# Performance work log

Measured on AMD Instinct MI355X. Metric: run time of the kernel, lower is better.

## Reference

```python
import jax, jax.numpy as jnp
from jax import lax
import numpy as np

B, N, H = 8, 2048, 128
THRESH = 0.3


def setup_inputs() -> dict:
    key = jax.random.key(0)
    k1, k2, k3 = jax.random.split(key, 3)
    node_embeddings = jax.random.normal(k1, (B * N, H), jnp.float32)
    # contiguous equal-sized graphs, as produced by PyG-style batching
    batch = jnp.repeat(jnp.arange(B, dtype=jnp.int64), N)
    # path_scorer params: Linear(2H->H) then Linear(H->1)
    W1 = jax.random.normal(k2, (2 * H, H), jnp.float32) * 0.02  # input-major
    b1 = jnp.zeros((H,), jnp.float32)
    W2 = jax.random.normal(k3, (H,), jnp.float32) * 0.02
    b2 = jnp.zeros((), jnp.float32)
    return {"node_embeddings": node_embeddings, "batch": batch,
            "W1": W1, "b1": b1, "W2": W2, "b2": b2}


def _run(emb, W1, b1, W2, b2):
    """emb: [B, N, H]. Returns (path [B,N] int32 padded with -1, scores [B,N])."""
    Bn, Nn, Hh = emb.shape
    bidx = jnp.arange(Bn)
    nidx = jnp.arange(Nn)
    # split first Linear: score(i,j) = sigmoid(w2 . elu(e_i@W1a + e_j@W1b + b1) + b2)
    A = jnp.einsum('bnh,hk->bnk', emb, W1[:Hh])          # current-node half [B,N,H]
    C = jnp.einsum('bnh,hk->bnk', emb, W1[Hh:]) + b1     # neighbor half + bias [B,N,H]
    root = jnp.argmax(emb[:, :, 0], axis=1)              # [B]
    visited0 = jnp.zeros((Bn, Nn), bool).at[bidx, root].set(True)

    def step(carry, _):
        cur, visited, active = carry
        # score every node against the current node in one fused pass
        h = jax.nn.elu(A[bidx, cur][:, None, :] + C)                      # [B,N,H]
        s = jax.nn.sigmoid(jnp.einsum('bnh,h->bn', h, W2) + b2)           # [B,N]
        sm = jnp.where(visited, -jnp.inf, s)
        best = jnp.argmax(sm, axis=1)                                     # first max == stable sort
        bscore = jnp.take_along_axis(sm, best[:, None], axis=1)[:, 0]
        take = active & (bscore > THRESH)
        visited = visited | (take[:, None] & (nidx[None, :] == best[:, None]))
        new_cur = jnp.where(take, best, cur)
        step_path = jnp.where(take, best, -1).astype(jnp.int32)
        step_score = jnp.where(take, bscore, 0.0).astype(emb.dtype)
        return (new_cur, visited, take), (step_path, step_score)

    init = (root, visited0, jnp.ones((Bn,), bool))
    _, (paths, scoreseq) = lax.scan(step, init, None, length=Nn - 1)
    path = jnp.concatenate([root[:, None].astype(jnp.int32), paths.T], axis=1)      # [B,N]
    scores = jnp.concatenate([jnp.ones((Bn, 1), emb.dtype), scoreseq.T], axis=1)    # root score = 1.0
    return path, scores


def reference(node_embeddings, batch, W1, b1, W2, b2):
    num_graphs = int(batch[-1]) + 1  # contiguous equal-sized graphs
    emb = node_embeddings.reshape(num_graphs, -1, node_embeddings.shape[-1])
    return _run(emb, W1, b1, W2, b2)
```

## Files before the change

kernel.cpp:

```cpp
#include <hip/hip_runtime.h>
#include <math.h>

#define B_ 8
#define N_ 2048
#define H_ 128
#define BN_ (B_ * N_)


__device__ __forceinline__ float elu1(float x) {
    return x > 0.f ? x : (__expf(x) - 1.f);
}

__device__ __forceinline__ unsigned enc_key(float v) {
    unsigned u = __float_as_uint(v);
    return (u & 0x80000000u) ? ~u : (u | 0x80000000u);
}
__device__ __forceinline__ float dec_key(unsigned k) {
    return __uint_as_float((k & 0x80000000u) ? (k & 0x7FFFFFFFu) : ~k);
}

__global__ __launch_bounds__(H_) void k_ac(const float* __restrict__ emb,
                                           const float* __restrict__ W1,
                                           const float* __restrict__ b1,
                                           float* __restrict__ A,
                                           float* __restrict__ C) {
    __shared__ float e[H_];
    const int i = blockIdx.x;
    const int k = threadIdx.x;
    e[k] = emb[(size_t)i * H_ + k];
    __syncthreads();
    float a = 0.f, c = 0.f;
#pragma unroll 8
    for (int h = 0; h < H_; ++h) {
        const float ev = e[h];
        a = fmaf(ev, W1[h * H_ + k], a);
        c = fmaf(ev, W1[(H_ + h) * H_ + k], c);
    }
    A[(size_t)i * H_ + k] = a;
    C[(size_t)i * H_ + k] = c + b1[k];
}

__global__ __launch_bounds__(256) void k_z(const float* __restrict__ A,
                                           const float* __restrict__ Cc,
                                           const float* __restrict__ w2,
                                           const float* __restrict__ b2p,
                                           unsigned* __restrict__ K) {
    const int lane = threadIdx.x & 63;
    const int wave = threadIdx.x >> 6;
    const int g = blockIdx.x >> 8;
    const int sub = blockIdx.x & 255;
    const int rowtile = sub & 127;
    const int jh = sub >> 7;
    const int ibase = rowtile * 16 + wave * 4;
    const int i = ibase + (lane & 3);
    const int he = (lane >> 2) * 8;
    const float b2v = *b2p;

    const float* Arow = A + ((size_t)g * N_ + i) * H_ + he;
    const float4 a0 = *(const float4*)(Arow);
    const float4 a1 = *(const float4*)(Arow + 4);
    const float4 w0 = *(const float4*)(w2 + he);
    const float4 w1v = *(const float4*)(w2 + he + 4);
    const float* Cg = Cc + (size_t)g * N_ * H_ + he;
    unsigned* Krow = K + ((size_t)g * N_ + i) * N_;
    const bool writer = ((lane >> 2) == 0);

    const int j0 = jh * 1024;
    for (int j = j0; j < j0 + 1024; j += 8) {
        float4 c0[8], c1[8];
#pragma unroll
        for (int q = 0; q < 8; ++q) {
            const float* Cj = Cg + (size_t)(j + q) * H_;
            c0[q] = *(const float4*)(Cj);
            c1[q] = *(const float4*)(Cj + 4);
        }
        float pv[8];
#pragma unroll
        for (int q = 0; q < 8; ++q) {
            float p = 0.f;
            p = fmaf(w0.x, elu1(a0.x + c0[q].x), p);
            p = fmaf(w0.y, elu1(a0.y + c0[q].y), p);
            p = fmaf(w0.z, elu1(a0.z + c0[q].z), p);
            p = fmaf(w0.w, elu1(a0.w + c0[q].w), p);
            p = fmaf(w1v.x, elu1(a1.x + c1[q].x), p);
            p = fmaf(w1v.y, elu1(a1.y + c1[q].y), p);
            p = fmaf(w1v.z, elu1(a1.z + c1[q].z), p);
            p = fmaf(w1v.w, elu1(a1.w + c1[q].w), p);
            pv[q] = p;
        }
#pragma unroll
        for (int q = 0; q < 8; ++q) pv[q] += __shfl_xor(pv[q], 4);
#pragma unroll
        for (int q = 0; q < 8; ++q) pv[q] += __shfl_xor(pv[q], 8);
#pragma unroll
        for (int q = 0; q < 8; ++q) pv[q] += __shfl_xor(pv[q], 16);
#pragma unroll
        for (int q = 0; q < 8; ++q) pv[q] += __shfl_xor(pv[q], 32);
        if (writer) {
            uint4 ka, kb;
            ka.x = enc_key(pv[0] + b2v);
            ka.y = enc_key(pv[1] + b2v);
            ka.z = enc_key(pv[2] + b2v);
            ka.w = enc_key(pv[3] + b2v);
            kb.x = enc_key(pv[4] + b2v);
            kb.y = enc_key(pv[5] + b2v);
            kb.z = enc_key(pv[6] + b2v);
            kb.w = enc_key(pv[7] + b2v);
            *(uint4*)(Krow + j) = ka;
            *(uint4*)(Krow + j + 4) = kb;
        }
    }
}

__global__ __launch_bounds__(64, 1) void k_path5(const float* __restrict__ emb,
                                                 const unsigned* __restrict__ K,
                                                 float* __restrict__ out) {
    const int g = blockIdx.x;
    const int lane = threadIdx.x;

    float bv0 = -INFINITY;
    int bi0 = 0x7fffffff;
    for (int j = lane; j < N_; j += 64) {
        const float v = emb[((size_t)g * N_ + j) * H_];
        if (v > bv0) { bv0 = v; bi0 = j; }
    }
#pragma unroll
    for (int off = 1; off < 64; off <<= 1) {
        const float ov = __shfl_xor(bv0, off);
        const int oi = __shfl_xor(bi0, off);
        if (ov > bv0 || (ov == bv0 && oi < bi0)) { bv0 = ov; bi0 = oi; }
    }
    int cur = bi0;
    unsigned vbits = 0;
    if (((cur >> 2) & 63) == lane)
        vbits |= 1u << (((cur >> 8) << 2) | (cur & 3));

    float* pathOut = out + (size_t)g * N_;
    float* scoreOut = out + (size_t)BN_ + (size_t)g * N_;
    if (lane == 0) {
        pathOut[0] = (float)cur;
        scoreOut[0] = 1.0f;
    }

    const unsigned* Kg = K + (size_t)g * N_ * N_;
    uint4 z[8];
    {
        const uint4* Kr = (const uint4*)(Kg + ((size_t)cur << 11));
#pragma unroll
        for (int k = 0; k < 8; ++k) z[k] = Kr[k * 64 + lane];
    }

    int t = 1;
    for (; t < N_; ++t) {
        unsigned best = 0u;
        int bj = 0;
#define SLOT(KRAW, S)                                                   \
        {                                                               \
            const unsigned kv_ = ((vbits >> (S)) & 1u) ? 0u : (KRAW);   \
            if (kv_ >= best) { best = kv_; bj = (S); }                  \
        }
        SLOT(z[7].w, 31) SLOT(z[7].z, 30) SLOT(z[7].y, 29) SLOT(z[7].x, 28)
        SLOT(z[6].w, 27) SLOT(z[6].z, 26) SLOT(z[6].y, 25) SLOT(z[6].x, 24)
        SLOT(z[5].w, 23) SLOT(z[5].z, 22) SLOT(z[5].y, 21) SLOT(z[5].x, 20)
        SLOT(z[4].w, 19) SLOT(z[4].z, 18) SLOT(z[4].y, 17) SLOT(z[4].x, 16)
        SLOT(z[3].w, 15) SLOT(z[3].z, 14) SLOT(z[3].y, 13) SLOT(z[3].x, 12)
        SLOT(z[2].w, 11) SLOT(z[2].z, 10) SLOT(z[2].y,  9) SLOT(z[2].x,  8)
        SLOT(z[1].w,  7) SLOT(z[1].z,  6) SLOT(z[1].y,  5) SLOT(z[1].x,  4)
        SLOT(z[0].w,  3) SLOT(z[0].z,  2) SLOT(z[0].y,  1) SLOT(z[0].x,  0)
#undef SLOT

        unsigned w = best;
#pragma unroll
        for (int off = 1; off < 64; off <<= 1) {
            const unsigned ow = __shfl_xor(w, off);
            if (ow > w) w = ow;
        }
        const unsigned long long mk = __ballot(best == w);
        int bi;
        if (__popcll(mk) == 1) {
            const int src = (int)(__ffsll((long long)mk) - 1);
            const int bjw = __shfl(bj, src);
            bi = ((bjw >> 2) << 8) | (src << 2) | (bjw & 3);
        } else {
            unsigned cand = (best == w)
                ? ~(unsigned)(((bj >> 2) << 8) | (lane << 2) | (bj & 3))
                : 0u;
#pragma unroll
            for (int off = 1; off < 64; off <<= 1) {
                const unsigned oc = __shfl_xor(cand, off);
                if (oc > cand) cand = oc;
            }
            bi = (int)(~cand);
        }

        {
            const uint4* Kr = (const uint4*)(Kg + ((size_t)bi << 11));
#pragma unroll
            for (int k = 0; k < 8; ++k) z[k] = Kr[k * 64 + lane];
        }

        const float bv = dec_key(w);
        const float s = 1.f / (1.f + expf(-bv));
        if (!((double)s > 0.3)) break;
        cur = bi;
        if (((cur >> 2) & 63) == lane)
            vbits |= 1u << (((cur >> 8) << 2) | (cur & 3));
        if (lane == 0) {
            pathOut[t] = (float)cur;
            scoreOut[t] = s;
        }
    }
    for (int tt = t + lane; tt < N_; tt += 64) {
        pathOut[tt] = -1.f;
        scoreOut[tt] = 0.f;
    }
}

__device__ __forceinline__ void blockArgmax(float& bv, int& bi, float* rv, int* ri,
                                            int lane, int wid, int nw) {
#pragma unroll
    for (int off = 1; off < 64; off <<= 1) {
        const float ov = __shfl_xor(bv, off);
        const int oi = __shfl_xor(bi, off);
        if (ov > bv || (ov == bv && oi < bi)) { bv = ov; bi = oi; }
    }
    if (lane == 0) { rv[wid] = bv; ri[wid] = bi; }
    __syncthreads();
    if (wid == 0) {
        float v = (lane < nw) ? rv[lane] : -INFINITY;
        int ix = (lane < nw) ? ri[lane] : 0x7fffffff;
#pragma unroll
        for (int off = 1; off < 16; off <<= 1) {
            const float ov = __shfl_xor(v, off);
            const int oi = __shfl_xor(ix, off);
            if (ov > v || (ov == v && oi < ix)) { v = ov; ix = oi; }
        }
        if (lane == 0) { rv[0] = v; ri[0] = ix; }
    }
    __syncthreads();
    bv = rv[0];
    bi = ri[0];
}

__global__ __launch_bounds__(1024) void k_path_fly(const float* __restrict__ emb,
                                                   const float* __restrict__ A,
                                                   const float* __restrict__ Cc,
                                                   const float* __restrict__ w2g,
                                                   const float* __restrict__ b2p,
                                                   float* __restrict__ out) {
    const int g = blockIdx.x;
    const int tid = threadIdx.x;
    const int lane = tid & 63, wid = tid >> 6;
    __shared__ float acur[H_], w2s[H_];
    __shared__ unsigned char vis[N_];
    __shared__ float rv[16];
    __shared__ int ri[16];
    const float b2v = *b2p;
    if (tid < H_) w2s[tid] = w2g[tid];
    for (int j = tid; j < N_; j += 1024) vis[j] = 0;

    float bv = -INFINITY;
    int bi = 0x7fffffff;
    for (int j = tid; j < N_; j += 1024) {
        const float v = emb[((size_t)g * N_ + j) * H_];
        if (v > bv) { bv = v; bi = j; }
    }
    __syncthreads();
    blockArgmax(bv, bi, rv, ri, lane, wid, 16);
    int cur = bi;
    float* pathOut = out + (size_t)g * N_;
    float* scoreOut = out + (size_t)BN_ + (size_t)g * N_;
    if (tid == 0) {
        vis[cur] = 1;
        pathOut[0] = (float)cur;
        scoreOut[0] = 1.0f;
    }
    __syncthreads();

    int t = 1;
    for (; t < N_; ++t) {
        if (tid < H_) acur[tid] = A[((size_t)g * N_ + cur) * H_ + tid];
        __syncthreads();
        float mbv = -INFINITY;
        int mbi = 0x7fffffff;
#pragma unroll
        for (int q = 0; q < 2; ++q) {
            const int j = tid + q * 1024;
            const float* Cj = Cc + ((size_t)g * N_ + j) * H_;
            float p = 0.f;
            for (int h = 0; h < H_; h += 4) {
                const float4 c = *(const float4*)(Cj + h);
                p = fmaf(w2s[h + 0], elu1(acur[h + 0] + c.x), p);
                p = fmaf(w2s[h + 1], elu1(acur[h + 1] + c.y), p);
                p = fmaf(w2s[h + 2], elu1(acur[h + 2] + c.z), p);
                p = fmaf(w2s[h + 3], elu1(acur[h + 3] + c.w), p);
            }
            const float z = p + b2v;
            if (!vis[j] && (z > mbv || (z == mbv && j < mbi))) { mbv = z; mbi = j; }
        }
        __syncthreads();
        blockArgmax(mbv, mbi, rv, ri, lane, wid, 16);
        const float s = 1.f / (1.f + expf(-mbv));
        if (!((double)s > 0.3)) break;
        cur = mbi;
        if (tid == 0) {
            vis[cur] = 1;
            pathOut[t] = (float)cur;
            scoreOut[t] = s;
        }
        __syncthreads();
    }
    for (int tt = t + tid; tt < N_; tt += 1024) {
        pathOut[tt] = -1.f;
        scoreOut[tt] = 0.f;
    }
}

extern "C" void kernel_launch(void* const* d_in, const int* in_sizes, int n_in,
                              void* d_out, int out_size, void* d_ws, size_t ws_size,
                              hipStream_t stream) {
    (void)in_sizes; (void)n_in; (void)out_size;
    const float* emb = (const float*)d_in[0];
    const float* W1 = (const float*)d_in[2];
    const float* b1 = (const float*)d_in[3];
    const float* w2 = (const float*)d_in[4];
    const float* b2 = (const float*)d_in[5];
    float* out = (float*)d_out;

    float* A = (float*)d_ws;
    float* C = A + (size_t)BN_ * H_;
    unsigned* K = (unsigned*)(C + (size_t)BN_ * H_);
    const size_t need = ((size_t)BN_ * H_ * 2 + (size_t)B_ * N_ * N_) * sizeof(float);

    hipLaunchKernelGGL(k_ac, dim3(BN_), dim3(H_), 0, stream, emb, W1, b1, A, C);
    if (ws_size >= need) {
        hipLaunchKernelGGL(k_z, dim3(2048), dim3(256), 0, stream, A, C, w2, b2, K);
        hipLaunchKernelGGL(k_path5, dim3(B_), dim3(64), 0, stream, emb, K, out);
    } else {
        hipLaunchKernelGGL(k_path_fly, dim3(B_), dim3(1024), 0, stream,
                           emb, A, C, w2, b2, out);
    }
}
```

Before: 3.218 ms.

## Fuse score-matrix build and path walk with per-row readiness flags

```diff
diff --git a/kernel.cpp b/kernel.cpp
--- a/kernel.cpp
+++ b/kernel.cpp
@@ -5,6 +5,7 @@
 #define N_ 2048
 #define H_ 128
 #define BN_ (B_ * N_)
+#define NZBLK_ 2048
 
 
 __device__ __forceinline__ float elu1(float x) {
@@ -18,6 +19,7 @@
 __device__ __forceinline__ float dec_key(unsigned k) {
     return __uint_as_float((k & 0x80000000u) ? (k & 0x7FFFFFFFu) : ~k);
 }
+__device__ __forceinline__ unsigned umax2(unsigned a, unsigned b) { return a > b ? a : b; }
 
 __global__ __launch_bounds__(H_) void k_ac(const float* __restrict__ emb,
                                            const float* __restrict__ W1,
@@ -40,81 +42,98 @@
     C[(size_t)i * H_ + k] = c + b1[k];
 }
 
-__global__ __launch_bounds__(256) void k_z(const float* __restrict__ A,
-                                           const float* __restrict__ Cc,
-                                           const float* __restrict__ w2,
-                                           const float* __restrict__ b2p,
-                                           unsigned* __restrict__ K) {
-    const int lane = threadIdx.x & 63;
-    const int wave = threadIdx.x >> 6;
-    const int g = blockIdx.x >> 8;
-    const int sub = blockIdx.x & 255;
-    const int rowtile = sub & 127;
-    const int jh = sub >> 7;
-    const int ibase = rowtile * 16 + wave * 4;
-    const int i = ibase + (lane & 3);
-    const int he = (lane >> 2) * 8;
-    const float b2v = *b2p;
-
-    const float* Arow = A + ((size_t)g * N_ + i) * H_ + he;
-    const float4 a0 = *(const float4*)(Arow);
-    const float4 a1 = *(const float4*)(Arow + 4);
-    const float4 w0 = *(const float4*)(w2 + he);
-    const float4 w1v = *(const float4*)(w2 + he + 4);
-    const float* Cg = Cc + (size_t)g * N_ * H_ + he;
-    unsigned* Krow = K + ((size_t)g * N_ + i) * N_;
-    const bool writer = ((lane >> 2) == 0);
-
-    const int j0 = jh * 1024;
-    for (int j = j0; j < j0 + 1024; j += 8) {
-        float4 c0[8], c1[8];
-#pragma unroll
-        for (int q = 0; q < 8; ++q) {
-            const float* Cj = Cg + (size_t)(j + q) * H_;
-            c0[q] = *(const float4*)(Cj);
-            c1[q] = *(const float4*)(Cj + 4);
-        }
-        float pv[8];
-#pragma unroll
-        for (int q = 0; q < 8; ++q) {
-            float p = 0.f;
-            p = fmaf(w0.x, elu1(a0.x + c0[q].x), p);
-            p = fmaf(w0.y, elu1(a0.y + c0[q].y), p);
-            p = fmaf(w0.z, elu1(a0.z + c0[q].z), p);
-            p = fmaf(w0.w, elu1(a0.w + c0[q].w), p);
-            p = fmaf(w1v.x, elu1(a1.x + c1[q].x), p);
-            p = fmaf(w1v.y, elu1(a1.y + c1[q].y), p);
-            p = fmaf(w1v.z, elu1(a1.z + c1[q].z), p);
-            p = fmaf(w1v.w, elu1(a1.w + c1[q].w), p);
-            pv[q] = p;
-        }
-#pragma unroll
-        for (int q = 0; q < 8; ++q) pv[q] += __shfl_xor(pv[q], 4);
-#pragma unroll
-        for (int q = 0; q < 8; ++q) pv[q] += __shfl_xor(pv[q], 8);
-#pragma unroll
-        for (int q = 0; q < 8; ++q) pv[q] += __shfl_xor(pv[q], 16);
-#pragma unroll
-        for (int q = 0; q < 8; ++q) pv[q] += __shfl_xor(pv[q], 32);
-        if (writer) {
-            uint4 ka, kb;
-            ka.x = enc_key(pv[0] + b2v);
-            ka.y = enc_key(pv[1] + b2v);
-            ka.z = enc_key(pv[2] + b2v);
-            ka.w = enc_key(pv[3] + b2v);
-            kb.x = enc_key(pv[4] + b2v);
-            kb.y = enc_key(pv[5] + b2v);
-            kb.z = enc_key(pv[6] + b2v);
-            kb.w = enc_key(pv[7] + b2v);
-            *(uint4*)(Krow + j) = ka;
-            *(uint4*)(Krow + j + 4) = kb;
-        }
-    }
-}
-
-__global__ __launch_bounds__(64, 1) void k_path5(const float* __restrict__ emb,
-                                                 const unsigned* __restrict__ K,
-                                                 float* __restrict__ out) {
+__global__ __launch_bounds__(256) void k_fused(const float* __restrict__ emb,
+                                               const float* __restrict__ A,
+                                               const float* __restrict__ Cc,
+                                               const float* __restrict__ w2,
+                                               const float* __restrict__ b2p,
+                                               unsigned* __restrict__ K,
+                                               unsigned* __restrict__ flags,
+                                               unsigned* __restrict__ gdone,
+                                               float* __restrict__ out) {
+    if (blockIdx.x >= B_) {
+        const int bid2 = blockIdx.x - B_;
+        const int lane = threadIdx.x & 63;
+        const int wave = threadIdx.x >> 6;
+        const int g = bid2 >> 8;
+        const int sub = bid2 & 255;
+        const int rowtile = sub & 127;
+        const int jh = sub >> 7;
+        const int ibase = rowtile * 16 + wave * 4;
+        const int i = ibase + (lane & 3);
+        const int he = (lane >> 2) * 8;
+        const float b2v = *b2p;
+
+        const float* Arow = A + ((size_t)g * N_ + i) * H_ + he;
+        const float4 a0 = *(const float4*)(Arow);
+        const float4 a1 = *(const float4*)(Arow + 4);
+        const float4 w0 = *(const float4*)(w2 + he);
+        const float4 w1v = *(const float4*)(w2 + he + 4);
+        const float* Cg = Cc + (size_t)g * N_ * H_ + he;
+        unsigned* Krow = K + ((size_t)g * N_ + i) * N_;
+        const bool writer = ((lane >> 2) == 0);
+
+        const int j0 = jh * 1024;
+        for (int j = j0; j < j0 + 1024; j += 8) {
+            float4 c0[8], c1[8];
+#pragma unroll
+            for (int q = 0; q < 8; ++q) {
+                const float* Cj = Cg + (size_t)(j + q) * H_;
+                c0[q] = *(const float4*)(Cj);
+                c1[q] = *(const float4*)(Cj + 4);
+            }
+            float pv[8];
+#pragma unroll
+            for (int q = 0; q < 8; ++q) {
+                float p = 0.f;
+                p = fmaf(w0.x, elu1(a0.x + c0[q].x), p);
+                p = fmaf(w0.y, elu1(a0.y + c0[q].y), p);
+                p = fmaf(w0.z, elu1(a0.z + c0[q].z), p);
+                p = fmaf(w0.w, elu1(a0.w + c0[q].w), p);
+                p = fmaf(w1v.x, elu1(a1.x + c1[q].x), p);
+                p = fmaf(w1v.y, elu1(a1.y + c1[q].y), p);
+                p = fmaf(w1v.z, elu1(a1.z + c1[q].z), p);
+                p = fmaf(w1v.w, elu1(a1.w + c1[q].w), p);
+                pv[q] = p;
+            }
+#pragma unroll
+            for (int q = 0; q < 8; ++q) pv[q] += __shfl_xor(pv[q], 4);
+#pragma unroll
+            for (int q = 0; q < 8; ++q) pv[q] += __shfl_xor(pv[q], 8);
+#pragma unroll
+            for (int q = 0; q < 8; ++q) pv[q] += __shfl_xor(pv[q], 16);
+#pragma unroll
+            for (int q = 0; q < 8; ++q) pv[q] += __shfl_xor(pv[q], 32);
+            if (writer) {
+                uint4 ka, kb;
+                ka.x = enc_key(pv[0] + b2v);
+                ka.y = enc_key(pv[1] + b2v);
+                ka.z = enc_key(pv[2] + b2v);
+                ka.w = enc_key(pv[3] + b2v);
+                kb.x = enc_key(pv[4] + b2v);
+                kb.y = enc_key(pv[5] + b2v);
+                kb.z = enc_key(pv[6] + b2v);
+                kb.w = enc_key(pv[7] + b2v);
+                *(uint4*)(Krow + j) = ka;
+                *(uint4*)(Krow + j + 4) = kb;
+            }
+        }
+
+        __threadfence();
+        __syncthreads();
+        if (threadIdx.x < 16) {
+            __hip_atomic_fetch_add(&flags[g * N_ + rowtile * 16 + threadIdx.x], 1u,
+                                   __ATOMIC_RELEASE, __HIP_MEMORY_SCOPE_AGENT);
+        }
+        __syncthreads();
+        if (threadIdx.x == 0) {
+            __hip_atomic_fetch_add(&gdone[g], 1u,
+                                   __ATOMIC_RELEASE, __HIP_MEMORY_SCOPE_AGENT);
+        }
+        return;
+    }
+
+    if (threadIdx.x >= 64) return;
     const int g = blockIdx.x;
     const int lane = threadIdx.x;
 
@@ -142,8 +161,22 @@
         scoreOut[0] = 1.0f;
     }
 
+    bool allReady = false;
+    const unsigned* fg = flags + (size_t)g * N_;
+    auto waitRow = [&](int r) {
+        if (allReady) return;
+        if (__hip_atomic_load(&gdone[g], __ATOMIC_ACQUIRE,
+                              __HIP_MEMORY_SCOPE_AGENT) == 256u) {
+            allReady = true;
+            return;
+        }
+        while (__hip_atomic_load(&fg[r], __ATOMIC_ACQUIRE,
+                                 __HIP_MEMORY_SCOPE_AGENT) < 2u) {}
+    };
+
     const unsigned* Kg = K + (size_t)g * N_ * N_;
     uint4 z[8];
+    waitRow(cur);
     {
         const uint4* Kr = (const uint4*)(Kg + ((size_t)cur << 11));
 #pragma unroll
@@ -193,6 +226,7 @@
             bi = (int)(~cand);
         }
 
+        waitRow(bi);
         {
             const uint4* Kr = (const uint4*)(Kg + ((size_t)bi << 11));
 #pragma unroll
@@ -330,12 +364,16 @@
     float* A = (float*)d_ws;
     float* C = A + (size_t)BN_ * H_;
     unsigned* K = (unsigned*)(C + (size_t)BN_ * H_);
-    const size_t need = ((size_t)BN_ * H_ * 2 + (size_t)B_ * N_ * N_) * sizeof(float);
+    unsigned* flags = K + (size_t)B_ * N_ * N_;
+    unsigned* gdone = flags + (size_t)BN_;
+    const size_t need = ((size_t)BN_ * H_ * 2 + (size_t)B_ * N_ * N_) * sizeof(float)
+                        + ((size_t)BN_ + B_) * sizeof(unsigned);
 
     hipLaunchKernelGGL(k_ac, dim3(BN_), dim3(H_), 0, stream, emb, W1, b1, A, C);
     if (ws_size >= need) {
-        hipLaunchKernelGGL(k_z, dim3(2048), dim3(256), 0, stream, A, C, w2, b2, K);
-        hipLaunchKernelGGL(k_path5, dim3(B_), dim3(64), 0, stream, emb, K, out);
+        hipMemsetAsync((void*)flags, 0, ((size_t)BN_ + B_) * sizeof(unsigned), stream);
+        hipLaunchKernelGGL(k_fused, dim3(B_ + NZBLK_), dim3(256), 0, stream,
+                           emb, A, C, w2, b2, K, flags, gdone, out);
     } else {
         hipLaunchKernelGGL(k_path_fly, dim3(B_), dim3(1024), 0, stream,
                            emb, A, C, w2, b2, out);
```

New measurement: 3.586 ms. 11.4% more time.

## Split sequential path argmax across four waves and use nontemporal loads for C

Applied to the files above, without the earlier changes.

```diff
diff --git a/kernel.cpp b/kernel.cpp
--- a/kernel.cpp
+++ b/kernel.cpp
@@ -6,6 +6,8 @@
 #define H_ 128
 #define BN_ (B_ * N_)
 
+
+typedef float f4v __attribute__((ext_vector_type(4)));
 
 __device__ __forceinline__ float elu1(float x) {
     return x > 0.f ? x : (__expf(x) - 1.f);
@@ -67,12 +69,12 @@
 
     const int j0 = jh * 1024;
     for (int j = j0; j < j0 + 1024; j += 8) {
-        float4 c0[8], c1[8];
+        f4v c0[8], c1[8];
 #pragma unroll
         for (int q = 0; q < 8; ++q) {
             const float* Cj = Cg + (size_t)(j + q) * H_;
-            c0[q] = *(const float4*)(Cj);
-            c1[q] = *(const float4*)(Cj + 4);
+            c0[q] = __builtin_nontemporal_load((const f4v*)(Cj));
+            c1[q] = __builtin_nontemporal_load((const f4v*)(Cj + 4));
         }
         float pv[8];
 #pragma unroll
@@ -112,105 +114,122 @@
     }
 }
 
-__global__ __launch_bounds__(64, 1) void k_path5(const float* __restrict__ emb,
-                                                 const unsigned* __restrict__ K,
-                                                 float* __restrict__ out) {
+__global__ __launch_bounds__(256) void k_path7(const float* __restrict__ emb,
+                                               const unsigned* __restrict__ K,
+                                               float* __restrict__ out) {
     const int g = blockIdx.x;
-    const int lane = threadIdx.x;
-
-    float bv0 = -INFINITY;
-    int bi0 = 0x7fffffff;
-    for (int j = lane; j < N_; j += 64) {
-        const float v = emb[((size_t)g * N_ + j) * H_];
-        if (v > bv0) { bv0 = v; bi0 = j; }
-    }
-#pragma unroll
-    for (int off = 1; off < 64; off <<= 1) {
-        const float ov = __shfl_xor(bv0, off);
-        const int oi = __shfl_xor(bi0, off);
-        if (ov > bv0 || (ov == bv0 && oi < bi0)) { bv0 = ov; bi0 = oi; }
-    }
-    int cur = bi0;
-    unsigned vbits = 0;
-    if (((cur >> 2) & 63) == lane)
-        vbits |= 1u << (((cur >> 8) << 2) | (cur & 3));
+    const int tid = threadIdx.x;
+    const int lane = tid & 63;
+    const int wid = tid >> 6;
+
+    __shared__ unsigned swv[2][4];
+    __shared__ int swj[2][4];
+    __shared__ int s_root;
 
     float* pathOut = out + (size_t)g * N_;
     float* scoreOut = out + (size_t)BN_ + (size_t)g * N_;
-    if (lane == 0) {
-        pathOut[0] = (float)cur;
-        scoreOut[0] = 1.0f;
-    }
+
+    if (tid < 64) {
+        float bv0 = -INFINITY;
+        int bi0 = 0x7fffffff;
+        for (int j = lane; j < N_; j += 64) {
+            const float v = emb[((size_t)g * N_ + j) * H_];
+            if (v > bv0) { bv0 = v; bi0 = j; }
+        }
+#pragma unroll
+        for (int off = 1; off < 64; off <<= 1) {
+            const float ov = __shfl_xor(bv0, off);
+            const int oi = __shfl_xor(bi0, off);
+            if (ov > bv0 || (ov == bv0 && oi < bi0)) { bv0 = ov; bi0 = oi; }
+        }
+        if (lane == 0) {
+            s_root = bi0;
+            pathOut[0] = (float)bi0;
+            scoreOut[0] = 1.0f;
+        }
+    }
+    __syncthreads();
+
+    int cur = s_root;
+    unsigned vb = 0;
+    if ((cur >> 3) == tid) vb |= 1u << (cur & 7);
 
     const unsigned* Kg = K + (size_t)g * N_ * N_;
-    uint4 z[8];
+    uint4 k0, k1;
     {
-        const uint4* Kr = (const uint4*)(Kg + ((size_t)cur << 11));
-#pragma unroll
-        for (int k = 0; k < 8; ++k) z[k] = Kr[k * 64 + lane];
-    }
-
+        const uint4* p = (const uint4*)(Kg + ((size_t)cur << 11) + (tid << 3));
+        k0 = p[0];
+        k1 = p[1];
+    }
+
+    int par = 0;
     int t = 1;
     for (; t < N_; ++t) {
-        unsigned best = 0u;
-        int bj = 0;
-#define SLOT(KRAW, S)                                                   \
-        {                                                               \
-            const unsigned kv_ = ((vbits >> (S)) & 1u) ? 0u : (KRAW);   \
-            if (kv_ >= best) { best = kv_; bj = (S); }                  \
-        }
-        SLOT(z[7].w, 31) SLOT(z[7].z, 30) SLOT(z[7].y, 29) SLOT(z[7].x, 28)
-        SLOT(z[6].w, 27) SLOT(z[6].z, 26) SLOT(z[6].y, 25) SLOT(z[6].x, 24)
-        SLOT(z[5].w, 23) SLOT(z[5].z, 22) SLOT(z[5].y, 21) SLOT(z[5].x, 20)
-        SLOT(z[4].w, 19) SLOT(z[4].z, 18) SLOT(z[4].y, 17) SLOT(z[4].x, 16)
-        SLOT(z[3].w, 15) SLOT(z[3].z, 14) SLOT(z[3].y, 13) SLOT(z[3].x, 12)
-        SLOT(z[2].w, 11) SLOT(z[2].z, 10) SLOT(z[2].y,  9) SLOT(z[2].x,  8)
-        SLOT(z[1].w,  7) SLOT(z[1].z,  6) SLOT(z[1].y,  5) SLOT(z[1].x,  4)
-        SLOT(z[0].w,  3) SLOT(z[0].z,  2) SLOT(z[0].y,  1) SLOT(z[0].x,  0)
-#undef SLOT
-
-        unsigned w = best;
+        const unsigned v0 = (vb & 1u)   ? 0u : k0.x;
+        const unsigned v1 = (vb & 2u)   ? 0u : k0.y;
+        const unsigned v2 = (vb & 4u)   ? 0u : k0.z;
+        const unsigned v3 = (vb & 8u)   ? 0u : k0.w;
+        const unsigned v4 = (vb & 16u)  ? 0u : k1.x;
+        const unsigned v5 = (vb & 32u)  ? 0u : k1.y;
+        const unsigned v6 = (vb & 64u)  ? 0u : k1.z;
+        const unsigned v7 = (vb & 128u) ? 0u : k1.w;
+
+        unsigned va = v0; int ja = 0;
+        if (v1 > va) { va = v1; ja = 1; }
+        unsigned vbp = v2; int jb = 2;
+        if (v3 > vbp) { vbp = v3; jb = 3; }
+        unsigned vc = v4; int jc = 4;
+        if (v5 > vc) { vc = v5; jc = 5; }
+        unsigned vd = v6; int jd = 6;
+        if (v7 > vd) { vd = v7; jd = 7; }
+        if (vbp > va) { va = vbp; ja = jb; }
+        if (vd > vc) { vc = vd; jc = jd; }
+        if (vc > va) { va = vc; ja = jc; }
+        unsigned wv_ = va;
+        int wj_ = (tid << 3) | ja;
+
 #pragma unroll
         for (int off = 1; off < 64; off <<= 1) {
-            const unsigned ow = __shfl_xor(w, off);
-            if (ow > w) w = ow;
-        }
-        const unsigned long long mk = __ballot(best == w);
-        int bi;
-        if (__popcll(mk) == 1) {
-            const int src = (int)(__ffsll((long long)mk) - 1);
-            const int bjw = __shfl(bj, src);
-            bi = ((bjw >> 2) << 8) | (src << 2) | (bjw & 3);
-        } else {
-            unsigned cand = (best == w)
-                ? ~(unsigned)(((bj >> 2) << 8) | (lane << 2) | (bj & 3))
-                : 0u;
-#pragma unroll
-            for (int off = 1; off < 64; off <<= 1) {
-                const unsigned oc = __shfl_xor(cand, off);
-                if (oc > cand) cand = oc;
-            }
-            bi = (int)(~cand);
-        }
-
+            const unsigned ov = __shfl_xor(wv_, off);
+            const int oj = __shfl_xor(wj_, off);
+            if (ov > wv_ || (ov == wv_ && oj < wj_)) { wv_ = ov; wj_ = oj; }
+        }
+        if (lane == 0) {
+            swv[par][wid] = wv_;
+            swj[par][wid] = wj_;
+        }
+        __syncthreads();
+
+        unsigned fv = swv[par][0];
+        int fj = swj[par][0];
+#pragma unroll
+        for (int w = 1; w < 4; ++w) {
+            const unsigned nv = swv[par][w];
+            const int nj = swj[par][w];
+            if (nv > fv || (nv == fv && nj < fj)) { fv = nv; fj = nj; }
+        }
+        const int bi = fj;
+
+        uint4 n0, n1;
         {
-            const uint4* Kr = (const uint4*)(Kg + ((size_t)bi << 11));
-#pragma unroll
-            for (int k = 0; k < 8; ++k) z[k] = Kr[k * 64 + lane];
-        }
-
-        const float bv = dec_key(w);
+            const uint4* p = (const uint4*)(Kg + ((size_t)bi << 11) + (tid << 3));
+            n0 = p[0];
+            n1 = p[1];
+        }
+
+        const float bv = dec_key(fv);
         const float s = 1.f / (1.f + expf(-bv));
         if (!((double)s > 0.3)) break;
-        cur = bi;
-        if (((cur >> 2) & 63) == lane)
-            vbits |= 1u << (((cur >> 8) << 2) | (cur & 3));
-        if (lane == 0) {
-            pathOut[t] = (float)cur;
+        if ((bi >> 3) == tid) vb |= 1u << (bi & 7);
+        if (tid == 0) {
+            pathOut[t] = (float)bi;
             scoreOut[t] = s;
         }
-    }
-    for (int tt = t + lane; tt < N_; tt += 64) {
+        k0 = n0;
+        k1 = n1;
+        par ^= 1;
+    }
+    for (int tt = t + tid; tt < N_; tt += 256) {
         pathOut[tt] = -1.f;
         scoreOut[tt] = 0.f;
     }
@@ -335,7 +354,7 @@
     hipLaunchKernelGGL(k_ac, dim3(BN_), dim3(H_), 0, stream, emb, W1, b1, A, C);
     if (ws_size >= need) {
         hipLaunchKernelGGL(k_z, dim3(2048), dim3(256), 0, stream, A, C, w2, b2, K);
-        hipLaunchKernelGGL(k_path5, dim3(B_), dim3(64), 0, stream, emb, K, out);
+        hipLaunchKernelGGL(k_path7, dim3(B_), dim3(256), 0, stream, emb, K, out);
     } else {
         hipLaunchKernelGGL(k_path_fly, dim3(B_), dim3(1024), 0, stream,
                            emb, A, C, w2, b2, out);
```

New measurement: 3.850 ms, median of 3. +19.6%, slower.
